# Optimization experiments

Measured on AMD Instinct MI355X. Metric: run time of the kernel, lower is better.

## Reference

```python
import jax, jax.numpy as jnp
import numpy as np

N, E, DIM = 50000, 500000, 64
EIN3, EIN4 = 16, 16

def setup_inputs() -> dict:
    key = jax.random.key(0)
    ks = jax.random.split(key, 8)
    x = jax.random.normal(ks[0], (N, DIM), dtype=jnp.float32)
    edge_index3 = jax.random.randint(ks[1], (2, E), 0, N, dtype=jnp.int64)
    edge_attr3 = jax.random.normal(ks[2], (E, EIN3), dtype=jnp.float32)
    edge_attr4 = jax.random.normal(ks[3], (E, EIN4), dtype=jnp.float32)
    batch = jnp.zeros((N,), dtype=jnp.int64)
    # MLP params: Linear(2*dim, 4*dim) -> ReLU -> Linear(4*dim, 1)
    W1 = jax.random.normal(ks[4], (2 * DIM, 4 * DIM), dtype=jnp.float32) / np.sqrt(2 * DIM)
    b1 = jnp.zeros((4 * DIM,), dtype=jnp.float32)
    W2 = jax.random.normal(ks[5], (4 * DIM, 1), dtype=jnp.float32) / np.sqrt(4 * DIM)
    b2 = jnp.zeros((1,), dtype=jnp.float32)
    return {"x": x, "edge_index3": edge_index3, "edge_attr3": edge_attr3,
            "edge_attr4": edge_attr4, "batch": batch,
            "W1": W1, "b1": b1, "W2": W2, "b2": b2}

def reference(x, edge_index3, edge_attr3, edge_attr4, batch, W1, b1, W2, b2):
    # gather endpoints: temp[k] = x[edge_index3[k]] -> [E, dim]
    src = x[edge_index3[0]]  # [E, dim]
    dst = x[edge_index3[1]]  # [E, dim]
    # symmetric concat: [[src|dst], [dst|src]] -> [2E, 2*dim]
    yhat = jnp.concatenate([
        jnp.concatenate([src, dst], axis=1),
        jnp.concatenate([dst, src], axis=1)], axis=0)
    h = jax.nn.relu(yhat @ W1 + b1)        # [2E, 4*dim]
    y = (h @ W2 + b2)[:, 0]                # [2E]
    return y.reshape(2, -1).mean(axis=0)   # [E]
```

## Files before the change

kernel.cpp:

```cpp
#include <hip/hip_runtime.h>

#define DIM 64
#define HID 256
#define ROWB 512
#define QSCALE  25.4f
#define DQSCALE (5.0f/127.0f)

typedef short s8v __attribute__((ext_vector_type(8)));
typedef float f4v __attribute__((ext_vector_type(4)));

union U16 { uint4 u; s8v s; };

__device__ __forceinline__ unsigned short bf16_rne(float f) {
    unsigned u = __float_as_uint(f);
    u = (u + 0x7fffu + ((u >> 16) & 1u)) >> 16;
    return (unsigned short)u;
}
__device__ __forceinline__ unsigned pk_bf16(float a, float b) {
    return (unsigned)bf16_rne(a) | ((unsigned)bf16_rne(b) << 16);
}

#define DPP_ADD(x, ctrl, rmask)                                               \
    (x) += __int_as_float(__builtin_amdgcn_update_dpp(                        \
        0, __float_as_int(x), (ctrl), (rmask), 0xf, true))
__device__ __forceinline__ float wave_sum64(float x) {
    DPP_ADD(x, 0x111, 0xf);
    DPP_ADD(x, 0x112, 0xf);
    DPP_ADD(x, 0x114, 0xf);
    DPP_ADD(x, 0x118, 0xf);
    DPP_ADD(x, 0x142, 0xa);
    DPP_ADD(x, 0x143, 0xc);
    return x;
}

__global__ __launch_bounds__(256) void prep_wfrag(
    const float* __restrict__ W1, unsigned short* __restrict__ wf)
{
    const int f = blockIdx.x * 256 + threadIdx.x;
    if (f >= 32 * 2 * 64) return;
    const int lane = f & 63;
    const int t    = (f >> 6) & 1;
    const int ct   = f >> 7;
    const int col  = ct * 16 + (lane & 15);
    const int k0   = t * 32 + (lane >> 4) * 8;
    const float* __restrict__ wsrc =
        W1 + ((col >= HID) ? (DIM * HID + col - HID) : col);
    unsigned short v[8];
#pragma unroll
    for (int j = 0; j < 8; ++j) v[j] = bf16_rne(wsrc[(size_t)(k0 + j) * HID]);
    uint4 o;
    o.x = (unsigned)v[0] | ((unsigned)v[1] << 16);
    o.y = (unsigned)v[2] | ((unsigned)v[3] << 16);
    o.z = (unsigned)v[4] | ((unsigned)v[5] << 16);
    o.w = (unsigned)v[6] | ((unsigned)v[7] << 16);
    *(uint4*)(wf + (size_t)f * 8) = o;
}

__global__ __launch_bounds__(256) void node_mfma_q(
    const float* __restrict__ x, const unsigned short* __restrict__ wf,
    const float* __restrict__ b1, unsigned char* __restrict__ tab, int n)
{
    const int lane    = threadIdx.x & 63;
    const int w       = threadIdx.x >> 6;
    const int rowgrp  = w >> 1;
    const int colhalf = w & 1;
    const int m       = lane & 15;
    const int quad    = lane >> 4;
    const int rbase   = blockIdx.x * 32 + rowgrp * 16;

    const int arow = rbase + m;
    const float* __restrict__ xr = x + (size_t)((arow < n) ? arow : (n - 1)) * DIM;
    s8v a[2];
#pragma unroll
    for (int t = 0; t < 2; ++t) {
        const float4 lo = *(const float4*)(xr + t * 32 + quad * 8);
        const float4 hi = *(const float4*)(xr + t * 32 + quad * 8 + 4);
        U16 u;
        u.u.x = pk_bf16(lo.x, lo.y);
        u.u.y = pk_bf16(lo.z, lo.w);
        u.u.z = pk_bf16(hi.x, hi.y);
        u.u.w = pk_bf16(hi.z, hi.w);
        a[t] = u.s;
    }

    const uint4* __restrict__ wfv = (const uint4*)wf;

    f4v acc[16];
#pragma unroll
    for (int ct = 0; ct < 16; ++ct) {
        const int ctg = colhalf * 16 + ct;
        U16 b0u, b1u;
        b0u.u = wfv[(ctg * 2 + 0) * 64 + lane];
        b1u.u = wfv[(ctg * 2 + 1) * 64 + lane];
        f4v c = {0.f, 0.f, 0.f, 0.f};
        c = __builtin_amdgcn_mfma_f32_16x16x32_bf16(a[0], b0u.s, c, 0, 0, 0);
        c = __builtin_amdgcn_mfma_f32_16x16x32_bf16(a[1], b1u.s, c, 0, 0, 0);
        if (colhalf == 0) {
            const float bias = b1[ctg * 16 + m];
            c[0] += bias; c[1] += bias; c[2] += bias; c[3] += bias;
        }
        acc[ct] = c;
    }

#pragma unroll
    for (int r = 0; r < 4; ++r) {
        const int gr = rbase + quad * 4 + r;
        if (gr >= n) continue;
        unsigned b[16];
#pragma unroll
        for (int ct = 0; ct < 16; ++ct) {
            float v = __builtin_rintf(acc[ct][r] * QSCALE);
            v = fminf(fmaxf(v, -127.f), 127.f);
            b[ct] = (unsigned)((int)v) & 255u;
        }
        uint4 o;
        o.x = b[0]  | (b[1]  << 8) | (b[2]  << 16) | (b[3]  << 24);
        o.y = b[4]  | (b[5]  << 8) | (b[6]  << 16) | (b[7]  << 24);
        o.z = b[8]  | (b[9]  << 8) | (b[10] << 16) | (b[11] << 24);
        o.w = b[12] | (b[13] << 8) | (b[14] << 16) | (b[15] << 24);
        *(uint4*)(tab + (size_t)gr * ROWB + colhalf * 256 + m * 16) = o;
    }
}

__global__ __launch_bounds__(256) void edge_mlp_q(
    const int* __restrict__ ei, const unsigned char* __restrict__ tab,
    const float* __restrict__ W2, const float* __restrict__ b2,
    float* __restrict__ out, int ne)
{
    const int lane = threadIdx.x & 63;
    const int lx   = lane ^ 32;
    const int wid  = blockIdx.x * (blockDim.x >> 6) + (threadIdx.x >> 6);
    const int nw   = gridDim.x * (blockDim.x >> 6);
    const int lp   = lane & 31;
    const int mcol = lp >> 1;
    const int ctb  = (lp & 1) * 8;
    float wv[8];
#pragma unroll
    for (int k = 0; k < 8; ++k) wv[k] = W2[(ctb + k) * 16 + mcol];
    const float bias = b2[0];

    for (int e0 = wid * 4; e0 < ne; e0 += nw * 4) {
        const int eu = __builtin_amdgcn_readfirstlane(e0);
        uint2 hs[4], hd[4];
#pragma unroll
        for (int q = 0; q < 4; ++q) {
            const int s = ei[eu + q];
            const int d = ei[ne + eu + q];
            hs[q] = *(const uint2*)(tab + (size_t)s * ROWB + 8 * lane);
            hd[q] = *(const uint2*)(tab + (size_t)d * ROWB + 8 * lx);
        }
        float p[4];
#pragma unroll
        for (int q = 0; q < 4; ++q) {
            float acc = 0.f;
#pragma unroll
            for (int k = 0; k < 4; ++k) {
                const int as = (int)(signed char)(hs[q].x >> (8 * k));
                const int bd = (int)(signed char)(hd[q].x >> (8 * k));
                const int t  = max(as + bd, 0);
                acc = fmaf((float)t, wv[k], acc);
            }
#pragma unroll
            for (int k = 0; k < 4; ++k) {
                const int as = (int)(signed char)(hs[q].y >> (8 * k));
                const int bd = (int)(signed char)(hd[q].y >> (8 * k));
                const int t  = max(as + bd, 0);
                acc = fmaf((float)t, wv[4 + k], acc);
            }
            p[q] = wave_sum64(acc);
        }
        if (lane == 63) {
            const float sc = 0.5f * DQSCALE;
            *(float4*)(out + e0) = make_float4(
                sc * p[0] + bias, sc * p[1] + bias,
                sc * p[2] + bias, sc * p[3] + bias);
        }
    }
}

extern "C" void kernel_launch(void* const* d_in, const int* in_sizes, int n_in,
                              void* d_out, int out_size, void* d_ws, size_t ws_size,
                              hipStream_t stream) {
    const float* x  = (const float*)d_in[0];
    const int*   ei = (const int*)d_in[1];
    const float* W1 = (const float*)d_in[5];
    const float* b1 = (const float*)d_in[6];
    const float* W2 = (const float*)d_in[7];
    const float* b2 = (const float*)d_in[8];
    float* out = (float*)d_out;

    const int n  = in_sizes[0] / DIM;
    const int ne = in_sizes[1] / 2;

    unsigned char*  tab = (unsigned char*)d_ws;
    unsigned short* wf  = (unsigned short*)(tab + (size_t)n * ROWB);

    prep_wfrag<<<16, 256, 0, stream>>>(W1, wf);
    node_mfma_q<<<(n + 31) / 32, 256, 0, stream>>>(x, wf, b1, tab, n);
    edge_mlp_q<<<8192, 256, 0, stream>>>(ei, tab, W2, b2, out, ne);
}
```

Baseline: 186.8 us.

## Process two edges per wave with 16-byte gathers, offset-encoded int8 and packed ops

The int8 node table now stores values offset by 127. The edge kernel can then compute relu(a+b) with packed unsigned 16-bit saturating subtraction, using byte permutes instead of sign-extending shifts. Each half-wave handles one edge using 16-byte loads, so a wave covers two edges per pass. The next pair's rows are prefetched while the current pair is computed, and each wave takes a contiguous block of 8-edge groups. The grid is cut to 2048 blocks with a tail path for leftover edges. This aims to reduce per-edge ALU work and gather instruction count, at the cost of extra registers for the prefetch and more complex edge indexing.

```diff
diff --git a/kernel.cpp b/kernel.cpp
--- a/kernel.cpp
+++ b/kernel.cpp
@@ -6,8 +6,10 @@
 #define QSCALE  25.4f
 #define DQSCALE (5.0f/127.0f)
 
-typedef short s8v __attribute__((ext_vector_type(8)));
-typedef float f4v __attribute__((ext_vector_type(4)));
+typedef short s8v  __attribute__((ext_vector_type(8)));
+typedef float f4v  __attribute__((ext_vector_type(4)));
+typedef float f2v  __attribute__((ext_vector_type(2)));
+typedef unsigned short u16x2 __attribute__((ext_vector_type(2)));
 
 union U16 { uint4 u; s8v s; };
 
@@ -20,18 +22,12 @@
     return (unsigned)bf16_rne(a) | ((unsigned)bf16_rne(b) << 16);
 }
 
+__device__ __forceinline__ u16x2 as_u16x2(unsigned v) { union { unsigned u; u16x2 s; } c; c.u = v; return c.s; }
+__device__ __forceinline__ unsigned as_u32(u16x2 v)   { union { u16x2 s; unsigned u; } c; c.s = v; return c.u; }
+
 #define DPP_ADD(x, ctrl, rmask)                                               \
     (x) += __int_as_float(__builtin_amdgcn_update_dpp(                        \
         0, __float_as_int(x), (ctrl), (rmask), 0xf, true))
-__device__ __forceinline__ float wave_sum64(float x) {
-    DPP_ADD(x, 0x111, 0xf);
-    DPP_ADD(x, 0x112, 0xf);
-    DPP_ADD(x, 0x114, 0xf);
-    DPP_ADD(x, 0x118, 0xf);
-    DPP_ADD(x, 0x142, 0xa);
-    DPP_ADD(x, 0x143, 0xc);
-    return x;
-}
 
 __global__ __launch_bounds__(256) void prep_wfrag(
     const float* __restrict__ W1, unsigned short* __restrict__ wf)
@@ -111,7 +107,7 @@
         for (int ct = 0; ct < 16; ++ct) {
             float v = __builtin_rintf(acc[ct][r] * QSCALE);
             v = fminf(fmaxf(v, -127.f), 127.f);
-            b[ct] = (unsigned)((int)v) & 255u;
+            b[ct] = (unsigned)((int)v + 127);
         }
         uint4 o;
         o.x = b[0]  | (b[1]  << 8) | (b[2]  << 16) | (b[3]  << 24);
@@ -122,58 +118,122 @@
     }
 }
 
-__global__ __launch_bounds__(256) void edge_mlp_q(
+__device__ __forceinline__ float pass_dot(const uint4 S, const uint4 D,
+                                          const f2v* __restrict__ w)
+{
+    const unsigned sa[4] = {S.x, S.y, S.z, S.w};
+    const unsigned da[4] = {D.x, D.y, D.z, D.w};
+    const u16x2 k254 = {254, 254};
+    f2v acc; acc.x = 0.f; acc.y = 0.f;
+#pragma unroll
+    for (int i = 0; i < 4; ++i) {
+        const unsigned zs0 = __builtin_amdgcn_perm(0u, sa[i], 0x0C010C00u);
+        const unsigned zs1 = __builtin_amdgcn_perm(0u, sa[i], 0x0C030C02u);
+        const unsigned zd0 = __builtin_amdgcn_perm(0u, da[i], 0x0C010C00u);
+        const unsigned zd1 = __builtin_amdgcn_perm(0u, da[i], 0x0C030C02u);
+        const unsigned r0 = as_u32(__builtin_elementwise_sub_sat(
+                                as_u16x2(zs0) + as_u16x2(zd0), k254));
+        const unsigned r1 = as_u32(__builtin_elementwise_sub_sat(
+                                as_u16x2(zs1) + as_u16x2(zd1), k254));
+        f2v f0, f1;
+        f0.x = (float)(r0 & 0xffu);
+        f0.y = (float)((r0 >> 16) & 0xffu);
+        f1.x = (float)(r1 & 0xffu);
+        f1.y = (float)((r1 >> 16) & 0xffu);
+        acc = f0 * w[2 * i] + acc;
+        acc = f1 * w[2 * i + 1] + acc;
+    }
+    return acc.x + acc.y;
+}
+
+__global__ __launch_bounds__(256, 8) void edge_mlp_q(
     const int* __restrict__ ei, const unsigned char* __restrict__ tab,
     const float* __restrict__ W2, const float* __restrict__ b2,
     float* __restrict__ out, int ne)
 {
     const int lane = threadIdx.x & 63;
-    const int lx   = lane ^ 32;
-    const int wid  = blockIdx.x * (blockDim.x >> 6) + (threadIdx.x >> 6);
-    const int nw   = gridDim.x * (blockDim.x >> 6);
-    const int lp   = lane & 31;
-    const int mcol = lp >> 1;
-    const int ctb  = (lp & 1) * 8;
-    float wv[8];
-#pragma unroll
-    for (int k = 0; k < 8; ++k) wv[k] = W2[(ctb + k) * 16 + mcol];
+    const int l31  = lane & 31;
+    const int m    = lane & 15;
+    const bool hi  = lane >= 32;
+
+    f2v w[8];
+#pragma unroll
+    for (int i = 0; i < 4; ++i) {
+        f2v w0, w1;
+        w0.x = W2[(4 * i + 0) * 16 + m]; w0.y = W2[(4 * i + 1) * 16 + m];
+        w1.x = W2[(4 * i + 2) * 16 + m]; w1.y = W2[(4 * i + 3) * 16 + m];
+        w[2 * i] = w0; w[2 * i + 1] = w1;
+    }
     const float bias = b2[0];
-
-    for (int e0 = wid * 4; e0 < ne; e0 += nw * 4) {
-        const int eu = __builtin_amdgcn_readfirstlane(e0);
-        uint2 hs[4], hd[4];
-#pragma unroll
-        for (int q = 0; q < 4; ++q) {
-            const int s = ei[eu + q];
-            const int d = ei[ne + eu + q];
-            hs[q] = *(const uint2*)(tab + (size_t)s * ROWB + 8 * lane);
-            hd[q] = *(const uint2*)(tab + (size_t)d * ROWB + 8 * lx);
-        }
-        float p[4];
-#pragma unroll
-        for (int q = 0; q < 4; ++q) {
-            float acc = 0.f;
-#pragma unroll
-            for (int k = 0; k < 4; ++k) {
-                const int as = (int)(signed char)(hs[q].x >> (8 * k));
-                const int bd = (int)(signed char)(hd[q].x >> (8 * k));
-                const int t  = max(as + bd, 0);
-                acc = fmaf((float)t, wv[k], acc);
+    const float sc   = 0.5f * DQSCALE;
+
+    const unsigned offS = 16u * (unsigned)l31;
+    const unsigned offD = 16u * (unsigned)(l31 ^ 16);
+
+    const int wflat = __builtin_amdgcn_readfirstlane(
+        (int)(blockIdx.x * 4 + (threadIdx.x >> 6)));
+    const int nw = (int)gridDim.x * 4;
+    const int ng = ne >> 3;
+    const int gq = ng / nw, gr = ng % nw;
+    int g        = wflat * gq + (wflat < gr ? wflat : gr);
+    const int ge = g + gq + (wflat < gr ? 1 : 0);
+
+    for (; g < ge; ++g) {
+        const int e0 = __builtin_amdgcn_readfirstlane(g << 3);
+        int se[8], de[8];
+#pragma unroll
+        for (int i = 0; i < 8; ++i) {
+            se[i] = ei[e0 + i];
+            de[i] = ei[ne + e0 + i];
+        }
+
+        uint4 S, D, Sn, Dn;
+        {
+            const unsigned vs = ((unsigned)(hi ? se[1] : se[0]) << 9) + offS;
+            const unsigned vd = ((unsigned)(hi ? de[1] : de[0]) << 9) + offD;
+            S = *(const uint4*)(tab + vs);
+            D = *(const uint4*)(tab + vd);
+        }
+#pragma unroll
+        for (int p = 0; p < 4; ++p) {
+            if (p < 3) {
+                const unsigned vs = ((unsigned)(hi ? se[2*p+3] : se[2*p+2]) << 9) + offS;
+                const unsigned vd = ((unsigned)(hi ? de[2*p+3] : de[2*p+2]) << 9) + offD;
+                Sn = *(const uint4*)(tab + vs);
+                Dn = *(const uint4*)(tab + vd);
             }
-#pragma unroll
-            for (int k = 0; k < 4; ++k) {
-                const int as = (int)(signed char)(hs[q].y >> (8 * k));
-                const int bd = (int)(signed char)(hd[q].y >> (8 * k));
-                const int t  = max(as + bd, 0);
-                acc = fmaf((float)t, wv[4 + k], acc);
+            float s = pass_dot(S, D, w);
+            DPP_ADD(s, 0x111, 0xf);
+            DPP_ADD(s, 0x112, 0xf);
+            DPP_ADD(s, 0x114, 0xf);
+            DPP_ADD(s, 0x118, 0xf);
+            DPP_ADD(s, 0x142, 0xa);
+            if (l31 == 31) out[e0 + 2 * p + (lane >> 5)] = fmaf(sc, s, bias);
+            S = Sn; D = Dn;
+        }
+    }
+
+    const int rem = ne & 7;
+    if (rem && wflat == 0) {
+        const int base = ne & ~7;
+#pragma unroll
+        for (int p = 0; p < 4; ++p) {
+            const int eA = base + 2 * p;
+            if (eA < ne) {
+                const int eB = (eA + 1 < ne) ? eA + 1 : eA;
+                const unsigned vs = ((unsigned)(hi ? ei[eB] : ei[eA]) << 9) + offS;
+                const unsigned vd = ((unsigned)(hi ? ei[ne + eB] : ei[ne + eA]) << 9) + offD;
+                const uint4 St = *(const uint4*)(tab + vs);
+                const uint4 Dt = *(const uint4*)(tab + vd);
+                float s = pass_dot(St, Dt, w);
+                DPP_ADD(s, 0x111, 0xf);
+                DPP_ADD(s, 0x112, 0xf);
+                DPP_ADD(s, 0x114, 0xf);
+                DPP_ADD(s, 0x118, 0xf);
+                DPP_ADD(s, 0x142, 0xa);
+                const int e = eA + (lane >> 5);
+                if (l31 == 31 && e < ne) out[e] = fmaf(sc, s, bias);
             }
-            p[q] = wave_sum64(acc);
-        }
-        if (lane == 63) {
-            const float sc = 0.5f * DQSCALE;
-            *(float4*)(out + e0) = make_float4(
-                sc * p[0] + bias, sc * p[1] + bias,
-                sc * p[2] + bias, sc * p[3] + bias);
         }
     }
 }
@@ -197,5 +257,5 @@
 
     prep_wfrag<<<16, 256, 0, stream>>>(W1, wf);
     node_mfma_q<<<(n + 31) / 32, 256, 0, stream>>>(x, wf, b1, tab, n);
-    edge_mlp_q<<<8192, 256, 0, stream>>>(ei, tab, W2, b2, out, ne);
-}
+    edge_mlp_q<<<2048, 256, 0, stream>>>(ei, tab, W2, b2, out, ne);
+}
```

Result: slower. 192.0 us (+2.8%).
